# Kernel optimization log

Measured on AMD Instinct MI355X. Metric: run time of the kernel, lower is better.

Reference implementation:

```python
import jax, jax.numpy as jnp
import numpy as np

B, S, H, HKV, D = 4, 1024, 32, 8, 128   # batch segments, seq per segment, q heads, kv heads, head dim
N = B * S                                # Ntotal (ragged tokens, equal-length segments)
SCALE = 1.0 / np.sqrt(D)                 # softmax_scale init kwarg
NEG = -1e9


def setup_inputs() -> dict:
    key = jax.random.key(0)
    kq, kk, kv = jax.random.split(key, 3)
    q = jax.random.normal(kq, (N, H, D), jnp.float32)
    k = jax.random.normal(kk, (N, HKV, D), jnp.float32)
    v = jax.random.normal(kv, (N, HKV, D), jnp.float32)
    # RoPE angles, rotate-half convention: concat(freqs, freqs), broadcast over heads
    inv_freq = 1.0 / (10000.0 ** (jnp.arange(D // 2, dtype=jnp.float32) / (D // 2)))
    pos = jnp.arange(S, dtype=jnp.float32)
    ang = pos[:, None] * inv_freq[None, :]                      # [S, D/2]
    idx_theta = jnp.tile(jnp.concatenate([ang, ang], -1), (B, 1))[:, None, :]  # [N,1,D]
    # per-segment causal mask, stacked -> [N, S]
    causal = jnp.where(jnp.arange(S)[None, :] <= jnp.arange(S)[:, None], 0.0, NEG).astype(jnp.float32)
    mask = jnp.tile(causal, (B, 1))
    return {"q": q, "k": k, "v": v, "idx_theta": idx_theta, "mask": mask}


def _rotate_half(x):
    # cat(-x[..., D/2:], x[..., :D/2])
    return jnp.concatenate([-x[..., D // 2:], x[..., : D // 2]], axis=-1)


def reference(q, k, v, idx_theta, mask):
    rep = H // HKV
    # repeat_kv: attention head i uses kv head i // rep (matches torch expand+reshape order)
    kx = jnp.repeat(k, rep, axis=1)                    # [N, H, D]
    vx = jnp.repeat(v, rep, axis=1)
    cos, sin = jnp.cos(idx_theta), jnp.sin(idx_theta)
    qr = q * cos + _rotate_half(q) * sin
    kr = kx * cos + _rotate_half(kx) * sin
    # segment-blocked attention (equal-length segments, vectorized over batch & heads)
    qb = qr.reshape(B, S, H, D)
    kb = kr.reshape(B, S, H, D)
    vb = vx.reshape(B, S, H, D)
    mb = mask.reshape(B, S, S)[:, None, :, :]          # [B,1,S,S]
    scores = jnp.einsum('bqhd,bkhd->bhqk', qb, kb) * SCALE + mb
    l = jax.nn.logsumexp(scores, axis=-1)              # [B,H,S] == max + logsumexp(shifted)
    p = jax.nn.softmax(scores, axis=-1)
    o = jnp.einsum('bhqk,bkhd->bqhd', p, vb)           # [B,S,H,D]
    o = o.reshape(N, H * D)                            # o.reshape(Ntotal, num_head, -1) flattened last two in torch is (N,H,D)->(N,H,D); original reshape(q.shape[0], q.shape[1], -1) keeps [N,H,D]
    o = o.reshape(N, H, D)
    l = l.transpose(0, 2, 1).reshape(N, H, 1)          # [Ntotal, num_head, 1]
    return o, l
```

## Files before the change

### kernel.cpp

```cpp
#include <hip/hip_runtime.h>

#define B_    4
#define S_    1024
#define H_    32
#define HKV_  8
#define D_    128
#define REP_  4
#define NTOT  (B_*S_)
#define QT_   64
#define KT_   32
#define KPAD  (KT_+8)
#define DPAD  (D_+8)

#define SCALE_ 0.08838834764831845f

typedef __attribute__((ext_vector_type(8))) short bf16x8;
typedef __attribute__((ext_vector_type(4))) float f32x4;
typedef __attribute__((ext_vector_type(4))) int   int4v;

__device__ __forceinline__ unsigned short f2bf(float f) {
    unsigned int u = __float_as_uint(f);
    u += 0x7FFFu + ((u >> 16) & 1u);
    return (unsigned short)(u >> 16);
}

__global__ void rope_k_kernel(const float* __restrict__ k,
                              const float* __restrict__ theta,
                              unsigned short* __restrict__ kr) {
    int t  = blockIdx.x * blockDim.x + threadIdx.x;
    int g  = t & 7;
    int hk = (t >> 3) & (HKV_ - 1);
    int n  = t >> 6;
    if (n >= NTOT) return;
    int d0 = g * 8;
    const float* kp = k + ((size_t)n * HKV_ + hk) * D_;
    const float* tp = theta + (size_t)n * D_;

    alignas(16) float kl[8], ku[8], thl[8], thu[8];
    *(float4*)&kl[0]  = *(const float4*)(kp + d0);
    *(float4*)&kl[4]  = *(const float4*)(kp + d0 + 4);
    *(float4*)&ku[0]  = *(const float4*)(kp + d0 + 64);
    *(float4*)&ku[4]  = *(const float4*)(kp + d0 + 68);
    *(float4*)&thl[0] = *(const float4*)(tp + d0);
    *(float4*)&thl[4] = *(const float4*)(tp + d0 + 4);
    *(float4*)&thu[0] = *(const float4*)(tp + d0 + 64);
    *(float4*)&thu[4] = *(const float4*)(tp + d0 + 68);

    alignas(16) unsigned short ol[8], ou[8];
#pragma unroll
    for (int j = 0; j < 8; ++j) {
        float sl, cl, su, cu;
        __sincosf(thl[j], &sl, &cl);
        __sincosf(thu[j], &su, &cu);
        ol[j] = f2bf(kl[j] * cl - ku[j] * sl);
        ou[j] = f2bf(ku[j] * cu + kl[j] * su);
    }
    unsigned short* outp = kr + ((size_t)n * HKV_ + hk) * D_;
    *(int4v*)(outp + d0)      = *(const int4v*)ol;
    *(int4v*)(outp + d0 + 64) = *(const int4v*)ou;
}

__global__ void vt_kernel(const float* __restrict__ v,
                          unsigned short* __restrict__ vt) {
    int t  = blockIdx.x * blockDim.x + threadIdx.x;
    int d  = t & (D_ - 1);
    int s8 = (t >> 7) & (S_/8 - 1);
    int hk = (t >> 14) & (HKV_ - 1);
    int b  = t >> 17;
    if (b >= B_) return;
    alignas(16) unsigned short out[8];
#pragma unroll
    for (int i = 0; i < 8; ++i) {
        int s = s8 * 8 + i;
        out[i] = f2bf(v[(((size_t)(b * S_ + s)) * HKV_ + hk) * D_ + d]);
    }
    *(int4v*)(vt + (((size_t)(b * HKV_ + hk)) * D_ + d) * S_ + s8 * 8) = *(const int4v*)out;
}

__global__ __launch_bounds__(256, 2)
void flash_kernel(const float* __restrict__ q,
                  const float* __restrict__ theta,
                  const unsigned short* __restrict__ kr,
                  const unsigned short* __restrict__ vt,
                  float* __restrict__ o_out,
                  float* __restrict__ l_out) {
    __shared__ unsigned short Ks[KT_][DPAD];
    __shared__ unsigned short Vs[D_][KPAD];
    __shared__ unsigned short Ps[4][16][KPAD];

    const int tid  = threadIdx.x;
    const int wave = tid >> 6;
    const int lane = tid & 63;
    const int l16  = lane & 15;
    const int quad = lane >> 4;

    const int bh = blockIdx.x;
    const int b  = bh >> 5;
    const int h  = bh & (H_ - 1);
    const int hk = h >> 2;
    const int nQT = S_ / QT_;
    const int qt = (nQT - 1) - blockIdx.y;
    const int qbase = qt * QT_;
    const int wq = qbase + wave * 16;

    bf16x8 qfrag[4];
    {
        const int n = b * S_ + wq + l16;
        const float* qp = q + ((size_t)n * H_ + h) * D_;
        const float* tp = theta + (size_t)n * D_;
#pragma unroll
        for (int c = 0; c < 4; ++c) {
            const int d0 = c * 32 + quad * 8;
            const int dp = d0 ^ 64;
            alignas(16) float qa[8], qb[8], th[8];
            *(float4*)&qa[0] = *(const float4*)(qp + d0);
            *(float4*)&qa[4] = *(const float4*)(qp + d0 + 4);
            *(float4*)&qb[0] = *(const float4*)(qp + dp);
            *(float4*)&qb[4] = *(const float4*)(qp + dp + 4);
            *(float4*)&th[0] = *(const float4*)(tp + d0);
            *(float4*)&th[4] = *(const float4*)(tp + d0 + 4);
            alignas(16) unsigned short tmp[8];
#pragma unroll
            for (int j = 0; j < 8; ++j) {
                float sv, cv;
                __sincosf(th[j], &sv, &cv);
                float rot = (d0 < 64) ? -qb[j] : qb[j];
                tmp[j] = f2bf(qa[j] * cv + rot * sv);
            }
            qfrag[c] = *(const bf16x8*)tmp;
        }
    }

    f32x4 acc[8];
#pragma unroll
    for (int dt = 0; dt < 8; ++dt) acc[dt] = (f32x4){0.f, 0.f, 0.f, 0.f};
    float m_st[4] = {-1e30f, -1e30f, -1e30f, -1e30f};
    float l_st[4] = {0.f, 0.f, 0.f, 0.f};

    const int n_kt = (qbase + QT_ - 1) / KT_ + 1;
    const int wq_hi = wq + 15;
    const size_t kbase  = (size_t)b * S_ * HKV_ * D_ + (size_t)hk * D_;
    const size_t vtbase = ((size_t)(b * HKV_ + hk)) * D_ * S_;

    for (int kt = 0; kt < n_kt; ++kt) {
        const int k0 = kt * KT_;
        __syncthreads();
#pragma unroll
        for (int u = tid; u < 512; u += 256) {
            int key = u >> 4;
            int d0  = (u & 15) * 8;
            int4v val = *(const int4v*)(kr + kbase + (size_t)(k0 + key) * HKV_ * D_ + d0);
            *(int4v*)(&Ks[key][d0]) = val;
        }
#pragma unroll
        for (int u = tid; u < 512; u += 256) {
            int d  = u >> 2;
            int kb = (u & 3) * 8;
            int4v val = *(const int4v*)(vt + vtbase + (size_t)d * S_ + k0 + kb);
            *(int4v*)(&Vs[d][kb]) = val;
        }
        __syncthreads();

        const bool active = (k0 <= wq_hi);
        if (active) {
            f32x4 c0 = (f32x4){0.f,0.f,0.f,0.f};
            f32x4 c1 = (f32x4){0.f,0.f,0.f,0.f};
#pragma unroll
            for (int c = 0; c < 4; ++c) {
                const int d0 = c * 32 + quad * 8;
                bf16x8 kb0 = *(const bf16x8*)(&Ks[l16][d0]);
                bf16x8 kb1 = *(const bf16x8*)(&Ks[l16 + 16][d0]);
                c0 = __builtin_amdgcn_mfma_f32_16x16x32_bf16(qfrag[c], kb0, c0, 0, 0, 0);
                c1 = __builtin_amdgcn_mfma_f32_16x16x32_bf16(qfrag[c], kb1, c1, 0, 0, 0);
            }
            const int key0 = k0 + l16, key1 = k0 + 16 + l16;
#pragma unroll
            for (int r = 0; r < 4; ++r) {
                const int qrow = wq + quad * 4 + r;
                float s0 = c0[r] * SCALE_;
                float s1 = c1[r] * SCALE_;
                if (key0 > qrow) s0 = -1e30f;
                if (key1 > qrow) s1 = -1e30f;
                float tmax = fmaxf(s0, s1);
                tmax = fmaxf(tmax, __shfl_xor(tmax, 1));
                tmax = fmaxf(tmax, __shfl_xor(tmax, 2));
                tmax = fmaxf(tmax, __shfl_xor(tmax, 4));
                tmax = fmaxf(tmax, __shfl_xor(tmax, 8));
                float mnew  = fmaxf(m_st[r], tmax);
                float alpha = __expf(m_st[r] - mnew);
                float p0 = __expf(s0 - mnew);
                float p1 = __expf(s1 - mnew);
                float rs = p0 + p1;
                rs += __shfl_xor(rs, 1);
                rs += __shfl_xor(rs, 2);
                rs += __shfl_xor(rs, 4);
                rs += __shfl_xor(rs, 8);
                l_st[r] = l_st[r] * alpha + rs;
                m_st[r] = mnew;
#pragma unroll
                for (int dt = 0; dt < 8; ++dt) acc[dt][r] *= alpha;
                Ps[wave][quad * 4 + r][l16]      = f2bf(p0);
                Ps[wave][quad * 4 + r][16 + l16] = f2bf(p1);
            }
        }
        __syncthreads();
        if (active) {
            bf16x8 pfrag = *(const bf16x8*)(&Ps[wave][l16][quad * 8]);
#pragma unroll
            for (int dt = 0; dt < 8; ++dt) {
                bf16x8 vfrag = *(const bf16x8*)(&Vs[dt * 16 + l16][quad * 8]);
                acc[dt] = __builtin_amdgcn_mfma_f32_16x16x32_bf16(pfrag, vfrag, acc[dt], 0, 0, 0);
            }
        }
    }

#pragma unroll
    for (int r = 0; r < 4; ++r) {
        const int qrow = wq + quad * 4 + r;
        const int n = b * S_ + qrow;
        const float inv = 1.0f / l_st[r];
        float* op = o_out + ((size_t)n * H_ + h) * D_;
#pragma unroll
        for (int dt = 0; dt < 8; ++dt)
            op[dt * 16 + l16] = acc[dt][r] * inv;
        if (l16 == 0)
            l_out[(size_t)n * H_ + h] = m_st[r] + logf(l_st[r]);
    }
}

extern "C" void kernel_launch(void* const* d_in, const int* in_sizes, int n_in,
                              void* d_out, int out_size, void* d_ws, size_t ws_size,
                              hipStream_t stream) {
    const float* q     = (const float*)d_in[0];
    const float* k     = (const float*)d_in[1];
    const float* v     = (const float*)d_in[2];
    const float* theta = (const float*)d_in[3];

    float* o_out = (float*)d_out;
    float* l_out = o_out + (size_t)NTOT * H_ * D_;

    unsigned short* kr = (unsigned short*)d_ws;
    unsigned short* vt = kr + (size_t)NTOT * HKV_ * D_;

    rope_k_kernel<<<(NTOT * HKV_ * 8) / 256, 256, 0, stream>>>(k, theta, kr);
    vt_kernel<<<(B_ * HKV_ * D_ * (S_ / 8)) / 256, 256, 0, stream>>>(v, vt);

    dim3 grid(B_ * H_, S_ / QT_);
    flash_kernel<<<grid, 256, 0, stream>>>(q, theta, kr, vt, o_out, l_out);
}
```

Measured before the change: 272.6 us.

## Transpose score MFMA to keep P in registers, enlarge key tile, tile V transpose

The flash kernel now computes S^T with K as the MFMA A operand. Each lane then holds a full query column of scores, so the softmax reduces mostly in registers and P feeds the PV MFMA (16x16x16) directly without an LDS round trip or an extra barrier. The key tile doubles to 64 with per-16 causal skipping, and launch bounds move to 4 blocks/SM. The V transpose kernel becomes an LDS-tiled, XOR-swizzled transpose with coalesced float4 reads. The risks are higher register pressure under the tighter launch bounds and the smaller-K MFMA for PV.

Result: faster. 240.7 us (-11.7%).

```diff
diff --git a/kernel.cpp b/kernel.cpp
--- a/kernel.cpp
+++ b/kernel.cpp
@@ -5,16 +5,16 @@
 #define H_    32
 #define HKV_  8
 #define D_    128
-#define REP_  4
 #define NTOT  (B_*S_)
 #define QT_   64
-#define KT_   32
+#define KT_   64
+#define DPAD  (D_+8)
 #define KPAD  (KT_+8)
-#define DPAD  (D_+8)
 
 #define SCALE_ 0.08838834764831845f
 
 typedef __attribute__((ext_vector_type(8))) short bf16x8;
+typedef __attribute__((ext_vector_type(4))) short bf16x4;
 typedef __attribute__((ext_vector_type(4))) float f32x4;
 typedef __attribute__((ext_vector_type(4))) int   int4v;
 
@@ -22,6 +22,9 @@
     unsigned int u = __float_as_uint(f);
     u += 0x7FFFu + ((u >> 16) & 1u);
     return (unsigned short)(u >> 16);
+}
+__device__ __forceinline__ unsigned int pack2bf(float a, float b) {
+    return (unsigned int)f2bf(a) | ((unsigned int)f2bf(b) << 16);
 }
 
 __global__ void rope_k_kernel(const float* __restrict__ k,
@@ -62,22 +65,40 @@
 
 __global__ void vt_kernel(const float* __restrict__ v,
                           unsigned short* __restrict__ vt) {
-    int t  = blockIdx.x * blockDim.x + threadIdx.x;
-    int d  = t & (D_ - 1);
-    int s8 = (t >> 7) & (S_/8 - 1);
-    int hk = (t >> 14) & (HKV_ - 1);
-    int b  = t >> 17;
-    if (b >= B_) return;
-    alignas(16) unsigned short out[8];
+    __shared__ unsigned short T[64][128];
+    int blk = blockIdx.x;
+    int s0  = (blk & (S_/64 - 1)) * 64;
+    int hk  = (blk >> 4) & (HKV_ - 1);
+    int b   = blk >> 7;
+    int tid = threadIdx.x;
+
 #pragma unroll
     for (int i = 0; i < 8; ++i) {
-        int s = s8 * 8 + i;
-        out[i] = f2bf(v[(((size_t)(b * S_ + s)) * HKV_ + hk) * D_ + d]);
-    }
-    *(int4v*)(vt + (((size_t)(b * HKV_ + hk)) * D_ + d) * S_ + s8 * 8) = *(const int4v*)out;
-}
-
-__global__ __launch_bounds__(256, 2)
+        int u  = tid + 256 * i;
+        int s  = u >> 5;
+        int G  = u & 31;
+        float4 val = *(const float4*)(v + (((size_t)(b * S_ + s0 + s)) * HKV_ + hk) * D_ + G * 4);
+        unsigned short* p = &T[s][(G ^ (s & 31)) * 4];
+        p[0] = f2bf(val.x); p[1] = f2bf(val.y); p[2] = f2bf(val.z); p[3] = f2bf(val.w);
+    }
+    __syncthreads();
+#pragma unroll
+    for (int i = 0; i < 4; ++i) {
+        int u = tid + 256 * i;
+        int d = u >> 3;
+        int g = u & 7;
+        int G = d >> 2;
+        alignas(16) unsigned short tmp[8];
+#pragma unroll
+        for (int j = 0; j < 8; ++j) {
+            int s = g * 8 + j;
+            tmp[j] = T[s][(G ^ (s & 31)) * 4 + (d & 3)];
+        }
+        *(int4v*)(vt + (((size_t)(b * HKV_ + hk)) * D_ + d) * S_ + s0 + g * 8) = *(const int4v*)tmp;
+    }
+}
+
+__global__ __launch_bounds__(256, 4)
 void flash_kernel(const float* __restrict__ q,
                   const float* __restrict__ theta,
                   const unsigned short* __restrict__ kr,
@@ -86,7 +107,6 @@
                   float* __restrict__ l_out) {
     __shared__ unsigned short Ks[KT_][DPAD];
     __shared__ unsigned short Vs[D_][KPAD];
-    __shared__ unsigned short Ps[4][16][KPAD];
 
     const int tid  = threadIdx.x;
     const int wave = tid >> 6;
@@ -98,14 +118,14 @@
     const int b  = bh >> 5;
     const int h  = bh & (H_ - 1);
     const int hk = h >> 2;
-    const int nQT = S_ / QT_;
-    const int qt = (nQT - 1) - blockIdx.y;
+    const int qt = (S_/QT_ - 1) - blockIdx.y;
     const int qbase = qt * QT_;
-    const int wq = qbase + wave * 16;
+    const int wq   = qbase + wave * 16;
+    const int qrow = wq + l16;
 
     bf16x8 qfrag[4];
     {
-        const int n = b * S_ + wq + l16;
+        const int n = b * S_ + qrow;
         const float* qp = q + ((size_t)n * H_ + h) * D_;
         const float* tp = theta + (size_t)n * D_;
 #pragma unroll
@@ -134,98 +154,122 @@
     f32x4 acc[8];
 #pragma unroll
     for (int dt = 0; dt < 8; ++dt) acc[dt] = (f32x4){0.f, 0.f, 0.f, 0.f};
-    float m_st[4] = {-1e30f, -1e30f, -1e30f, -1e30f};
-    float l_st[4] = {0.f, 0.f, 0.f, 0.f};
-
-    const int n_kt = (qbase + QT_ - 1) / KT_ + 1;
-    const int wq_hi = wq + 15;
-    const size_t kbase  = (size_t)b * S_ * HKV_ * D_ + (size_t)hk * D_;
-    const size_t vtbase = ((size_t)(b * HKV_ + hk)) * D_ * S_;
-
+    float m_st = -1e30f, l_st = 0.f;
+
+    const unsigned short* kseg = kr + ((size_t)b * S_ * HKV_ + hk) * D_;
+    const unsigned short* vseg = vt + ((size_t)(b * HKV_ + hk)) * D_ * S_;
+
+    const int n_kt = qt + 1;
     for (int kt = 0; kt < n_kt; ++kt) {
         const int k0 = kt * KT_;
         __syncthreads();
 #pragma unroll
-        for (int u = tid; u < 512; u += 256) {
-            int key = u >> 4;
-            int d0  = (u & 15) * 8;
-            int4v val = *(const int4v*)(kr + kbase + (size_t)(k0 + key) * HKV_ * D_ + d0);
-            *(int4v*)(&Ks[key][d0]) = val;
-        }
-#pragma unroll
-        for (int u = tid; u < 512; u += 256) {
-            int d  = u >> 2;
-            int kb = (u & 3) * 8;
-            int4v val = *(const int4v*)(vt + vtbase + (size_t)d * S_ + k0 + kb);
-            *(int4v*)(&Vs[d][kb]) = val;
+        for (int i = 0; i < 4; ++i) {
+            int u = tid + 256 * i;
+            int key = u >> 4, g = u & 15;
+            *(int4v*)&Ks[key][g * 8] =
+                *(const int4v*)(kseg + (size_t)(k0 + key) * (HKV_ * D_) + g * 8);
+        }
+#pragma unroll
+        for (int i = 0; i < 4; ++i) {
+            int u = tid + 256 * i;
+            int d = u >> 3, g = u & 7;
+            *(int4v*)&Vs[d][g * 8] =
+                *(const int4v*)(vseg + (size_t)d * S_ + k0 + g * 8);
         }
         __syncthreads();
 
-        const bool active = (k0 <= wq_hi);
-        if (active) {
-            f32x4 c0 = (f32x4){0.f,0.f,0.f,0.f};
-            f32x4 c1 = (f32x4){0.f,0.f,0.f,0.f};
-#pragma unroll
-            for (int c = 0; c < 4; ++c) {
-                const int d0 = c * 32 + quad * 8;
-                bf16x8 kb0 = *(const bf16x8*)(&Ks[l16][d0]);
-                bf16x8 kb1 = *(const bf16x8*)(&Ks[l16 + 16][d0]);
-                c0 = __builtin_amdgcn_mfma_f32_16x16x32_bf16(qfrag[c], kb0, c0, 0, 0, 0);
-                c1 = __builtin_amdgcn_mfma_f32_16x16x32_bf16(qfrag[c], kb1, c1, 0, 0, 0);
-            }
-            const int key0 = k0 + l16, key1 = k0 + 16 + l16;
+        int nact = (wq + 15 - k0) / 16 + 1;
+        if (nact > 4) nact = 4;
+
+        f32x4 sc[4];
+#pragma unroll
+        for (int kc = 0; kc < 4; ++kc) {
+            if (kc < nact) {
+                f32x4 c = (f32x4){0.f, 0.f, 0.f, 0.f};
+#pragma unroll
+                for (int cc = 0; cc < 4; ++cc) {
+                    bf16x8 kf = *(const bf16x8*)&Ks[kc * 16 + l16][cc * 32 + quad * 8];
+                    c = __builtin_amdgcn_mfma_f32_16x16x32_bf16(kf, qfrag[cc], c, 0, 0, 0);
+                }
+                sc[kc] = c;
+            }
+        }
+
+        float s[16];
+#pragma unroll
+        for (int kc = 0; kc < 4; ++kc) {
 #pragma unroll
             for (int r = 0; r < 4; ++r) {
-                const int qrow = wq + quad * 4 + r;
-                float s0 = c0[r] * SCALE_;
-                float s1 = c1[r] * SCALE_;
-                if (key0 > qrow) s0 = -1e30f;
-                if (key1 > qrow) s1 = -1e30f;
-                float tmax = fmaxf(s0, s1);
-                tmax = fmaxf(tmax, __shfl_xor(tmax, 1));
-                tmax = fmaxf(tmax, __shfl_xor(tmax, 2));
-                tmax = fmaxf(tmax, __shfl_xor(tmax, 4));
-                tmax = fmaxf(tmax, __shfl_xor(tmax, 8));
-                float mnew  = fmaxf(m_st[r], tmax);
-                float alpha = __expf(m_st[r] - mnew);
-                float p0 = __expf(s0 - mnew);
-                float p1 = __expf(s1 - mnew);
-                float rs = p0 + p1;
-                rs += __shfl_xor(rs, 1);
-                rs += __shfl_xor(rs, 2);
-                rs += __shfl_xor(rs, 4);
-                rs += __shfl_xor(rs, 8);
-                l_st[r] = l_st[r] * alpha + rs;
-                m_st[r] = mnew;
-#pragma unroll
-                for (int dt = 0; dt < 8; ++dt) acc[dt][r] *= alpha;
-                Ps[wave][quad * 4 + r][l16]      = f2bf(p0);
-                Ps[wave][quad * 4 + r][16 + l16] = f2bf(p1);
-            }
-        }
-        __syncthreads();
-        if (active) {
-            bf16x8 pfrag = *(const bf16x8*)(&Ps[wave][l16][quad * 8]);
-#pragma unroll
-            for (int dt = 0; dt < 8; ++dt) {
-                bf16x8 vfrag = *(const bf16x8*)(&Vs[dt * 16 + l16][quad * 8]);
-                acc[dt] = __builtin_amdgcn_mfma_f32_16x16x32_bf16(pfrag, vfrag, acc[dt], 0, 0, 0);
-            }
-        }
-    }
-
-#pragma unroll
-    for (int r = 0; r < 4; ++r) {
-        const int qrow = wq + quad * 4 + r;
-        const int n = b * S_ + qrow;
-        const float inv = 1.0f / l_st[r];
-        float* op = o_out + ((size_t)n * H_ + h) * D_;
-#pragma unroll
-        for (int dt = 0; dt < 8; ++dt)
-            op[dt * 16 + l16] = acc[dt][r] * inv;
-        if (l16 == 0)
-            l_out[(size_t)n * H_ + h] = m_st[r] + logf(l_st[r]);
-    }
+                int key = k0 + kc * 16 + quad * 4 + r;
+                s[kc * 4 + r] = (kc < nact && key <= qrow) ? sc[kc][r] * SCALE_ : -1e30f;
+            }
+        }
+        float tmax = s[0];
+#pragma unroll
+        for (int i = 1; i < 16; ++i) tmax = fmaxf(tmax, s[i]);
+        tmax = fmaxf(tmax, __shfl_xor(tmax, 16));
+        tmax = fmaxf(tmax, __shfl_xor(tmax, 32));
+        float mnew  = fmaxf(m_st, tmax);
+        float alpha = __expf(m_st - mnew);
+
+        unsigned int pk[8];
+        float rs = 0.f;
+#pragma unroll
+        for (int kc = 0; kc < 4; ++kc) {
+            float p0 = __expf(s[kc * 4 + 0] - mnew);
+            float p1 = __expf(s[kc * 4 + 1] - mnew);
+            float p2 = __expf(s[kc * 4 + 2] - mnew);
+            float p3 = __expf(s[kc * 4 + 3] - mnew);
+            rs += (p0 + p1) + (p2 + p3);
+            pk[kc * 2 + 0] = pack2bf(p0, p1);
+            pk[kc * 2 + 1] = pack2bf(p2, p3);
+        }
+        rs += __shfl_xor(rs, 16);
+        rs += __shfl_xor(rs, 32);
+        l_st = l_st * alpha + rs;
+        m_st = mnew;
+#pragma unroll
+        for (int dt = 0; dt < 8; ++dt) {
+            acc[dt][0] *= alpha; acc[dt][1] *= alpha;
+            acc[dt][2] *= alpha; acc[dt][3] *= alpha;
+        }
+
+#pragma unroll
+        for (int kc = 0; kc < 4; ++kc) {
+            if (kc < nact) {
+                union { unsigned int u[2]; bf16x4 v; } pb;
+                pb.u[0] = pk[kc * 2 + 0];
+                pb.u[1] = pk[kc * 2 + 1];
+#if __has_builtin(__builtin_amdgcn_mfma_f32_16x16x16bf16_1k)
+#pragma unroll
+                for (int dt = 0; dt < 8; ++dt) {
+                    bf16x4 vf = *(const bf16x4*)&Vs[dt * 16 + l16][kc * 16 + quad * 4];
+                    acc[dt] = __builtin_amdgcn_mfma_f32_16x16x16bf16_1k(vf, pb.v, acc[dt], 0, 0, 0);
+                }
+#else
+                bf16x8 pb8 = (bf16x8){pb.v[0], pb.v[1], pb.v[2], pb.v[3], 0, 0, 0, 0};
+#pragma unroll
+                for (int dt = 0; dt < 8; ++dt) {
+                    bf16x4 vf = *(const bf16x4*)&Vs[dt * 16 + l16][kc * 16 + quad * 4];
+                    bf16x8 vf8 = (bf16x8){vf[0], vf[1], vf[2], vf[3], 0, 0, 0, 0};
+                    acc[dt] = __builtin_amdgcn_mfma_f32_16x16x32_bf16(vf8, pb8, acc[dt], 0, 0, 0);
+                }
+#endif
+            }
+        }
+    }
+
+    const float inv = 1.0f / l_st;
+    const int n = b * S_ + qrow;
+    float* op = o_out + ((size_t)n * H_ + h) * D_;
+#pragma unroll
+    for (int dt = 0; dt < 8; ++dt) {
+        float4 o4 = {acc[dt][0] * inv, acc[dt][1] * inv, acc[dt][2] * inv, acc[dt][3] * inv};
+        *(float4*)(op + dt * 16 + quad * 4) = o4;
+    }
+    if (quad == 0)
+        l_out[(size_t)n * H_ + h] = m_st + logf(l_st);
 }
 
 extern "C" void kernel_launch(void* const* d_in, const int* in_sizes, int n_in,
@@ -243,7 +287,7 @@
     unsigned short* vt = kr + (size_t)NTOT * HKV_ * D_;
 
     rope_k_kernel<<<(NTOT * HKV_ * 8) / 256, 256, 0, stream>>>(k, theta, kr);
-    vt_kernel<<<(B_ * HKV_ * D_ * (S_ / 8)) / 256, 256, 0, stream>>>(v, vt);
+    vt_kernel<<<B_ * HKV_ * (S_ / 64), 256, 0, stream>>>(v, vt);
 
     dim3 grid(B_ * H_, S_ / QT_);
     flash_kernel<<<grid, 256, 0, stream>>>(q, theta, kr, vt, o_out, l_out);
```
